# Performance work log

Measured on AMD Instinct MI355X. Metric: run time of the kernel, lower is better.

## Reference

```python
import jax, jax.numpy as jnp
import numpy as np

B, S, D = 2, 2048, 1024
N_HEADS, D_HEAD = 16, 64
INIT_STD = 0.02


def setup_inputs() -> dict:
    key = jax.random.key(0)
    k_res, k_q, k_k, k_v, k_o = jax.random.split(key, 5)
    residual = jax.random.normal(k_res, (B, S, D), dtype=jnp.float32)
    W_Q = INIT_STD * jax.random.normal(k_q, (N_HEADS, D_HEAD, D), dtype=jnp.float32)
    W_K = INIT_STD * jax.random.normal(k_k, (N_HEADS, D_HEAD, D), dtype=jnp.float32)
    W_V = INIT_STD * jax.random.normal(k_v, (N_HEADS, D_HEAD, D), dtype=jnp.float32)
    W_O = INIT_STD * jax.random.normal(k_o, (N_HEADS, D_HEAD, D), dtype=jnp.float32)
    return {"residual": residual, "W_Q": W_Q, "W_K": W_K, "W_V": W_V, "W_O": W_O}


def reference(residual, W_Q, W_K, W_V, W_O):
    seq_len = residual.shape[1]
    # projections: [b, n, p, h]  (heads first, matching q.transpose(1,2))
    q = jnp.einsum('bpd,nhd->bnph', residual, W_Q)
    k = jnp.einsum('bpd,nhd->bnph', residual, W_K)
    v = jnp.einsum('bpd,nhd->bnph', residual, W_V)
    scale = 1.0 / jnp.sqrt(jnp.asarray(q.shape[-1], dtype=residual.dtype))
    # [b, n, p_q, p_k] full score matrix (faithful to original naive impl)
    scores = jnp.einsum('bnqh,bnkh->bnqk', q, k) * scale
    causal = jnp.tril(jnp.ones((seq_len, seq_len), dtype=bool))
    scores = jnp.where(causal, scores, -jnp.inf)
    pattern = jax.nn.softmax(scores, axis=-1)
    attn_out = jnp.einsum('bnqk,bnkh->bnqh', pattern, v)
    # output projection summed over heads: 'bpnh,nhd->bpd'
    return jnp.einsum('bnph,nhd->bpd', attn_out, W_O)
```

## Files before the change

### kernel.cpp

```cpp
#include <hip/hip_runtime.h>
#include <math.h>


#define SS_ 2048
#define DD_ 1024
#define NH_ 16
#define BN_ 32
#define BS_ 4096

typedef __bf16 bf16x8 __attribute__((ext_vector_type(8)));
typedef __bf16 bf16x4 __attribute__((ext_vector_type(4)));
typedef short shortx4 __attribute__((ext_vector_type(4)));
typedef float floatx4 __attribute__((ext_vector_type(4)));
typedef unsigned short ushortx4 __attribute__((ext_vector_type(4)));

__device__ __forceinline__ unsigned short f2bf(float f) {
    union { float f; unsigned u; } v; v.f = f;
    unsigned r = v.u + 0x7FFFu + ((v.u >> 16) & 1u);
    return (unsigned short)(r >> 16);
}

__device__ __forceinline__ floatx4 mfma_pv(bf16x4 a, bf16x4 b, floatx4 c) {
#if __has_builtin(__builtin_amdgcn_mfma_f32_16x16x16_bf16)
    return __builtin_amdgcn_mfma_f32_16x16x16_bf16(a, b, c, 0, 0, 0);
#else
    return __builtin_amdgcn_mfma_f32_16x16x16bf16_1k(
        __builtin_bit_cast(shortx4, a), __builtin_bit_cast(shortx4, b), c, 0, 0, 0);
#endif
}

__device__ __forceinline__ void gl_lds16(const unsigned short* g, unsigned short* l) {
    __builtin_amdgcn_global_load_lds(
        (const __attribute__((address_space(1))) unsigned int*)g,
        (__attribute__((address_space(3))) unsigned int*)l, 16, 0, 0);
}

__global__ __launch_bounds__(256) void cast_bf16_kernel(
    const float* __restrict__ resid, const float* __restrict__ WQ,
    const float* __restrict__ WK, const float* __restrict__ WV,
    unsigned short* __restrict__ residB, unsigned short* __restrict__ WQb,
    unsigned short* __restrict__ WKb, unsigned short* __restrict__ WVb)
{
    const int x = blockIdx.x;
    int z, ix;
    if (x < 4096) { z = 0; ix = x; }
    else { z = 1 + ((x - 4096) >> 10); ix = (x - 4096) & 1023; }
    const float* src = (z == 0) ? resid : (z == 1) ? WQ : (z == 2) ? WK : WV;
    unsigned short* dst = (z == 0) ? residB : (z == 1) ? WQb : (z == 2) ? WKb : WVb;
    const int i = (ix * 256 + threadIdx.x) * 4;
    float4 f = *(const float4*)(src + i);
    ushortx4 o;
    o[0] = f2bf(f.x); o[1] = f2bf(f.y); o[2] = f2bf(f.z); o[3] = f2bf(f.w);
    *(ushortx4*)(dst + i) = o;
}

__global__ __launch_bounds__(256) void wo_transpose_kernel(
    const float* __restrict__ WO, unsigned short* __restrict__ WOt)
{
    __shared__ float t[64][65];
    const int kk0 = blockIdx.x * 64, d0 = blockIdx.y * 64;
    #pragma unroll
    for (int it = 0; it < 16; ++it) {
        int idx = it * 256 + threadIdx.x;
        int r = idx >> 6, c = idx & 63;
        t[r][c] = WO[(kk0 + r) * DD_ + d0 + c];
    }
    __syncthreads();
    #pragma unroll
    for (int it = 0; it < 16; ++it) {
        int idx = it * 256 + threadIdx.x;
        int r = idx >> 6, c = idx & 63;
        WOt[(d0 + r) * DD_ + kk0 + c] = f2bf(t[c][r]);
    }
}

__global__ __launch_bounds__(512, 4) void qkv_fused_kernel(
    const unsigned short* __restrict__ residB,
    const unsigned short* __restrict__ WQb,
    const unsigned short* __restrict__ WKb,
    const unsigned short* __restrict__ WVb,
    unsigned short* __restrict__ q, unsigned short* __restrict__ kk,
    unsigned short* __restrict__ vT)
{
    __shared__ unsigned short As[128 * 64];
    __shared__ unsigned short Bq[64 * 64];
    __shared__ unsigned short Bk[64 * 64];
    __shared__ unsigned short Bv[64 * 64];
    const int tid = threadIdx.x;
    const int l = tid & 63, w = tid >> 6;
    const int quad = l >> 4, lan = l & 15;
    const int mBase = blockIdx.x * 128;
    const int head = blockIdx.y;
    const int nBase = head * 64;

    floatx4 accQ[4], accK[4], accV[4];
    #pragma unroll
    for (int ni = 0; ni < 4; ++ni)
        #pragma unroll
        for (int i = 0; i < 4; ++i) {
            accQ[ni][i] = 0.f; accK[ni][i] = 0.f; accV[ni][i] = 0.f;
        }

    const int sr = l >> 3;
    const int sgx = ((l & 7) ^ sr) * 8;

    for (int k0 = 0; k0 < DD_; k0 += 64) {
        __syncthreads();
        gl_lds16(residB + (size_t)(mBase + w * 16 + sr) * DD_ + k0 + sgx,
                 As + (w * 16) * 64);
        gl_lds16(residB + (size_t)(mBase + w * 16 + 8 + sr) * DD_ + k0 + sgx,
                 As + (w * 16 + 8) * 64);
        gl_lds16(WQb + (size_t)(nBase + w * 8 + sr) * DD_ + k0 + sgx,
                 Bq + (w * 8) * 64);
        gl_lds16(WKb + (size_t)(nBase + w * 8 + sr) * DD_ + k0 + sgx,
                 Bk + (w * 8) * 64);
        gl_lds16(WVb + (size_t)(nBase + w * 8 + sr) * DD_ + k0 + sgx,
                 Bv + (w * 8) * 64);
        __syncthreads();
        #pragma unroll
        for (int ks = 0; ks < 2; ++ks) {
            const int fo = (((ks * 4 + quad) ^ (lan & 7)) << 3);
            bf16x8 a = *(const bf16x8*)(As + (w * 16 + lan) * 64 + fo);
            bf16x8 bq[4], bk[4], bv[4];
            #pragma unroll
            for (int ni = 0; ni < 4; ++ni) {
                bq[ni] = *(const bf16x8*)(Bq + (ni * 16 + lan) * 64 + fo);
                bk[ni] = *(const bf16x8*)(Bk + (ni * 16 + lan) * 64 + fo);
                bv[ni] = *(const bf16x8*)(Bv + (ni * 16 + lan) * 64 + fo);
            }
            #pragma unroll
            for (int ni = 0; ni < 4; ++ni) {
                accQ[ni] = __builtin_amdgcn_mfma_f32_16x16x32_bf16(a, bq[ni], accQ[ni], 0, 0, 0);
                accK[ni] = __builtin_amdgcn_mfma_f32_16x16x32_bf16(a, bk[ni], accK[ni], 0, 0, 0);
                accV[ni] = __builtin_amdgcn_mfma_f32_16x16x32_bf16(a, bv[ni], accV[ni], 0, 0, 0);
            }
        }
    }
    const int m0 = mBase + w * 16 + quad * 4;
    const int bb = m0 >> 11, ss0 = m0 & 2047;
    const float scl = 0.125f * 1.44269504088896340736f;
    #pragma unroll
    for (int ni = 0; ni < 4; ++ni) {
        const int h = ni * 16 + lan;
        bf16x4 obq, obv;
        #pragma unroll
        for (int reg = 0; reg < 4; ++reg) {
            obq[reg] = static_cast<__bf16>(accQ[ni][reg] * scl);
            obv[reg] = static_cast<__bf16>(accV[ni][reg]);
        }
        *(bf16x4*)(q  + ((size_t)(bb * NH_ + head) * 64 + h) * SS_ + ss0) = obq;
        *(bf16x4*)(vT + ((size_t)(bb * NH_ + head) * 64 + h) * SS_ + ss0) = obv;
        #pragma unroll
        for (int reg = 0; reg < 4; ++reg)
            kk[((size_t)(bb * NH_ + head) * SS_ + ss0 + reg) * 64 + h] =
                f2bf(accK[ni][reg]);
    }
}

__global__ __launch_bounds__(256, 4) void flash_mfma_kernel(
    const unsigned short* __restrict__ q,
    const unsigned short* __restrict__ k,
    const unsigned short* __restrict__ vT,
    unsigned short* __restrict__ attn)
{
    __shared__ unsigned short ldsK[2][64 * 64];
    __shared__ unsigned short ldsV[2][64 * 64];
    const int l = threadIdx.x & 63, w = threadIdx.x >> 6;
    const int quad = l >> 4, lan = l & 15;
    const int f = blockIdx.x;
    const int bn = (f & 7) | (((f >> 3) & 3) << 3);
    const int g = f >> 5;
    const int ch = (g < 8) ? (31 - g)
                 : (g < 16) ? (g + 8)
                 : (g < 24) ? (15 - (g - 16))
                 : (g - 24);

    const unsigned short* Qg = q  + (size_t)bn * 64 * SS_;
    const unsigned short* Kg = k  + (size_t)bn * SS_ * 64;
    const unsigned short* Vg = vT + (size_t)bn * 64 * SS_;

    const int srl = l >> 3;
    const int sgx = (l & 7) ^ srl;

    const int qRow0 = ch * 64 + w * 16;
    const int qAbs = qRow0 + lan;

    bf16x8 Qf0, Qf1;
    #pragma unroll
    for (int j = 0; j < 8; ++j) {
        Qf0[j] = *(const __bf16*)(Qg + (size_t)(quad * 8 + j) * SS_ + qAbs);
        Qf1[j] = *(const __bf16*)(Qg + (size_t)(quad * 8 + j + 32) * SS_ + qAbs);
    }

    bf16x4 ones;
    #pragma unroll
    for (int i = 0; i < 4; ++i) ones[i] = static_cast<__bf16>(1.0f);

    float mrow = -INFINITY;
    floatx4 l_acc;
    floatx4 o[4];
    #pragma unroll
    for (int i = 0; i < 4; ++i) l_acc[i] = 0.f;
    #pragma unroll
    for (int t = 0; t < 4; ++t)
        #pragma unroll
        for (int i = 0; i < 4; ++i) o[t][i] = 0.f;

    #define STAGE_K(kt_, buf_)                                                  \
        { const int row0_ = w * 16, kB_ = (kt_) * 64;                           \
          gl_lds16(Kg + (size_t)(kB_ + row0_ + srl) * 64 + sgx * 8,             \
                   &ldsK[buf_][row0_ * 64]);                                    \
          gl_lds16(Kg + (size_t)(kB_ + row0_ + 8 + srl) * 64 + sgx * 8,         \
                   &ldsK[buf_][(row0_ + 8) * 64]); }
    #define STAGE_V(kt_, buf_)                                                  \
        { const int row0_ = w * 16, kB_ = (kt_) * 64;                           \
          gl_lds16(Vg + (size_t)(row0_ + srl) * SS_ + kB_ + sgx * 8,            \
                   &ldsV[buf_][row0_ * 64]);                                    \
          gl_lds16(Vg + (size_t)(row0_ + 8 + srl) * SS_ + kB_ + sgx * 8,        \
                   &ldsV[buf_][(row0_ + 8) * 64]); }
    #define QK_TILE(dst_, buf_)                                                 \
        { const unsigned short* Kb_ = &ldsK[buf_][0];                           \
          bf16x8 K0v_[4], K1v_[4];                                              \
          _Pragma("unroll")                                                     \
          for (int nt = 0; nt < 4; ++nt) {                                      \
              const unsigned short* kr_ = Kb_ + (nt * 16 + lan) * 64;           \
              K0v_[nt] = *(const bf16x8*)(kr_ + ((quad ^ (lan & 7)) << 3));     \
              K1v_[nt] = *(const bf16x8*)(kr_ + (((quad + 4) ^ (lan & 7)) << 3)); } \
          _Pragma("unroll")                                                     \
          for (int nt = 0; nt < 4; ++nt) {                                      \
              floatx4 zz_; zz_[0] = zz_[1] = zz_[2] = zz_[3] = 0.f;             \
              dst_[nt] = __builtin_amdgcn_mfma_f32_16x16x32_bf16(K0v_[nt], Qf0, zz_, 0, 0, 0); \
              dst_[nt] = __builtin_amdgcn_mfma_f32_16x16x32_bf16(K1v_[nt], Qf1, dst_[nt], 0, 0, 0); } }

    STAGE_K(0, 0);
    STAGE_V(0, 0);
    __syncthreads();
    if (ch >= 1) STAGE_K(1, 1);
    floatx4 scCur[4], scNext[4];
    QK_TILE(scCur, 0);

    for (int kt = 0; kt <= ch; ++kt) {
        const int kBase = kt * 64;
        __syncthreads();
        if (kt + 2 <= ch) STAGE_K(kt + 2, (kt + 2) & 1);
        if (kt + 1 <= ch) {
            STAGE_V(kt + 1, (kt + 1) & 1);
            QK_TILE(scNext, (kt + 1) & 1);
        }
        const unsigned short* Vb = &ldsV[kt & 1][0];
        bf16x4 Vfv[4][4];
        #pragma unroll
        for (int t = 0; t < 4; ++t) {
            const unsigned short* vr = Vb + (t * 16 + lan) * 64 + ((quad & 1) << 2);
            #pragma unroll
            for (int nt = 0; nt < 4; ++nt) {
                const int g2 = nt * 2 + (quad >> 1);
                Vfv[t][nt] = *(const bf16x4*)(vr + ((g2 ^ (lan & 7)) << 3));
            }
        }
        if (kt == ch) {
            #pragma unroll
            for (int nt = 0; nt < 4; ++nt)
                #pragma unroll
                for (int reg = 0; reg < 4; ++reg)
                    if (kBase + nt * 16 + quad * 4 + reg > qAbs)
                        scCur[nt][reg] = -INFINITY;
        }
        float mx = scCur[0][0];
        #pragma unroll
        for (int nt = 0; nt < 4; ++nt)
            #pragma unroll
            for (int reg = 0; reg < 4; ++reg) mx = fmaxf(mx, scCur[nt][reg]);
        mx = fmaxf(mx, __shfl_xor(mx, 16, 64));
        mx = fmaxf(mx, __shfl_xor(mx, 32, 64));
        const float mnew = fmaxf(mrow, mx);
        if (!__all(mx <= mrow)) {
            const float alpha = exp2f(mrow - mnew);
            l_acc[0] *= alpha;
            #pragma unroll
            for (int t = 0; t < 4; ++t)
                #pragma unroll
                for (int i = 0; i < 4; ++i) o[t][i] *= alpha;
        }
        mrow = mnew;
        bf16x4 pb[4];
        #pragma unroll
        for (int nt = 0; nt < 4; ++nt)
            #pragma unroll
            for (int reg = 0; reg < 4; ++reg)
                pb[nt][reg] = static_cast<__bf16>(exp2f(scCur[nt][reg] - mnew));
        #pragma unroll
        for (int nt = 0; nt < 4; ++nt)
            l_acc = mfma_pv(ones, pb[nt], l_acc);
        #pragma unroll
        for (int t = 0; t < 4; ++t)
            #pragma unroll
            for (int nt = 0; nt < 4; ++nt)
                o[t] = mfma_pv(Vfv[t][nt], pb[nt], o[t]);
        #pragma unroll
        for (int nt = 0; nt < 4; ++nt) scCur[nt] = scNext[nt];
    }
    const float rl = 1.f / l_acc[0];
    #pragma unroll
    for (int t = 0; t < 4; ++t) {
        bf16x4 ob;
        #pragma unroll
        for (int reg = 0; reg < 4; ++reg)
            ob[reg] = static_cast<__bf16>(o[t][reg] * rl);
        *(bf16x4*)(attn + ((size_t)bn * SS_ + qAbs) * 64 + t * 16 + quad * 4) = ob;
    }
    #undef STAGE_K
    #undef STAGE_V
    #undef QK_TILE
}

__global__ __launch_bounds__(256) void out_m97_kernel(
    const unsigned short* __restrict__ attn,
    const unsigned short* __restrict__ WOt,
    float* __restrict__ out)
{
    __shared__ unsigned short As[64 * 64];
    __shared__ unsigned short Bs[128 * 64];
    const int tid = threadIdx.x;
    const int l = tid & 63, w = tid >> 6;
    const int quad = l >> 4, lan = l & 15;
    const int mBase = blockIdx.x * 64;
    const int nBase = blockIdx.y * 128;
    const int wm = (w & 1) * 32, wn = (w >> 1) * 64;
    const int bbU = mBase >> 11;
    const int ssBase = mBase & 2047;

    floatx4 acc[2][4];
    #pragma unroll
    for (int a = 0; a < 2; ++a)
        #pragma unroll
        for (int b = 0; b < 4; ++b)
            #pragma unroll
            for (int i = 0; i < 4; ++i) acc[a][b][i] = 0.f;

    const int sr = l >> 3;
    const int sgx = ((l & 7) ^ sr) * 8;

    for (int kt = 0; kt < 16; ++kt) {
        const int k0 = kt * 64;
        __syncthreads();
        #pragma unroll
        for (int i = 0; i < 2; ++i) {
            const int row = i * 32 + w * 8 + sr;
            gl_lds16(attn + ((size_t)(bbU * NH_ + kt) * SS_ + ssBase + row) * 64 + sgx,
                     As + i * 2048 + w * 512);
        }
        #pragma unroll
        for (int i = 0; i < 4; ++i) {
            const int row = i * 32 + w * 8 + sr;
            gl_lds16(WOt + (size_t)(nBase + row) * DD_ + k0 + sgx,
                     Bs + i * 2048 + w * 512);
        }
        __syncthreads();
        #pragma unroll
        for (int ks = 0; ks < 2; ++ks) {
            const int fo = (((ks * 4 + quad) ^ (lan & 7)) << 3);
            bf16x8 a[2], b[4];
            #pragma unroll
            for (int mi = 0; mi < 2; ++mi)
                a[mi] = *(const bf16x8*)(As + (wm + mi * 16 + lan) * 64 + fo);
            #pragma unroll
            for (int ni = 0; ni < 4; ++ni)
                b[ni] = *(const bf16x8*)(Bs + (wn + ni * 16 + lan) * 64 + fo);
            #pragma unroll
            for (int mi = 0; mi < 2; ++mi)
                #pragma unroll
                for (int ni = 0; ni < 4; ++ni)
                    acc[mi][ni] = __builtin_amdgcn_mfma_f32_16x16x32_bf16(
                        a[mi], b[ni], acc[mi][ni], 0, 0, 0);
        }
    }
    #pragma unroll
    for (int mi = 0; mi < 2; ++mi)
        #pragma unroll
        for (int ni = 0; ni < 4; ++ni)
            #pragma unroll
            for (int reg = 0; reg < 4; ++reg) {
                int m = mBase + wm + mi * 16 + quad * 4 + reg;
                out[(size_t)m * DD_ + nBase + wn + ni * 16 + lan] = acc[mi][ni][reg];
            }
}

extern "C" void kernel_launch(void* const* d_in, const int* in_sizes, int n_in,
                              void* d_out, int out_size, void* d_ws, size_t ws_size,
                              hipStream_t stream) {
    const float* resid = (const float*)d_in[0];
    const float* WQ    = (const float*)d_in[1];
    const float* WK    = (const float*)d_in[2];
    const float* WV    = (const float*)d_in[3];
    const float* WO    = (const float*)d_in[4];
    float* out = (float*)d_out;

    unsigned short* q      = (unsigned short*)d_ws;
    unsigned short* kk     = q      + 4194304;
    unsigned short* vT     = kk     + 4194304;
    unsigned short* attn   = vT     + 4194304;
    unsigned short* residB = attn   + 4194304;
    unsigned short* WQb    = residB + 4194304;
    unsigned short* WKb    = WQb    + 1048576;
    unsigned short* WVb    = WKb    + 1048576;
    unsigned short* WOt    = WVb    + 1048576;

    cast_bf16_kernel<<<dim3(7168), 256, 0, stream>>>(
        resid, WQ, WK, WV, residB, WQb, WKb, WVb);
    wo_transpose_kernel<<<dim3(16, 16), 256, 0, stream>>>(WO, WOt);
    qkv_fused_kernel<<<dim3(32, 16), 512, 0, stream>>>(
        residB, WQb, WKb, WVb, q, kk, vT);
    flash_mfma_kernel<<<dim3(1024), dim3(256), 0, stream>>>(q, kk, vT, attn);
    out_m97_kernel<<<dim3(64, 8), 256, 0, stream>>>(attn, WOt, out);
}
```

Baseline: 178.8 us.

## Split flash-attention KV range across two wave groups and merge softmax states

Each flash-attention block now runs 512 threads as two groups of four waves. Each group processes half of the causal key tiles for the same 64 query rows, using separate double-buffered LDS for K and V. A final merge step passes the running max, denominator and output accumulators through LDS and combines them in the log-sum-exp way. This shortens the serial loop for long-context blocks and improves load balance. The cost is double the LDS, extra synchronisation and merge overhead, and a dropped launch-bounds occupancy hint.

```diff
diff --git a/kernel.cpp b/kernel.cpp
--- a/kernel.cpp
+++ b/kernel.cpp
@@ -157,15 +157,16 @@
     }
 }
 
-__global__ __launch_bounds__(256, 4) void flash_mfma_kernel(
+__global__ __launch_bounds__(512) void flash_mfma_kernel(
     const unsigned short* __restrict__ q,
     const unsigned short* __restrict__ k,
     const unsigned short* __restrict__ vT,
     unsigned short* __restrict__ attn)
 {
-    __shared__ unsigned short ldsK[2][64 * 64];
-    __shared__ unsigned short ldsV[2][64 * 64];
+    __shared__ unsigned short ldsBuf[2][2][2][64 * 64];
     const int l = threadIdx.x & 63, w = threadIdx.x >> 6;
+    const int grp = w >> 2;
+    const int wl = w & 3;
     const int quad = l >> 4, lan = l & 15;
     const int f = blockIdx.x;
     const int bn = (f & 7) | (((f >> 3) & 3) << 3);
@@ -182,8 +183,12 @@
     const int srl = l >> 3;
     const int sgx = (l & 7) ^ srl;
 
-    const int qRow0 = ch * 64 + w * 16;
-    const int qAbs = qRow0 + lan;
+    const int qAbs = ch * 64 + wl * 16 + lan;
+
+    const int half = (ch + 1) >> 1;
+    const int base = grp ? half : 0;
+    const int cg   = grp ? (ch + 1 - half) : half;
+    const int nIt  = ch + 1 - half;
 
     bf16x8 Qf0, Qf1;
     #pragma unroll
@@ -207,19 +212,19 @@
         for (int i = 0; i < 4; ++i) o[t][i] = 0.f;
 
     #define STAGE_K(kt_, buf_)                                                  \
-        { const int row0_ = w * 16, kB_ = (kt_) * 64;                           \
+        { const int row0_ = wl * 16, kB_ = (kt_) * 64;                          \
           gl_lds16(Kg + (size_t)(kB_ + row0_ + srl) * 64 + sgx * 8,             \
-                   &ldsK[buf_][row0_ * 64]);                                    \
+                   &ldsBuf[grp][0][buf_][row0_ * 64]);                          \
           gl_lds16(Kg + (size_t)(kB_ + row0_ + 8 + srl) * 64 + sgx * 8,         \
-                   &ldsK[buf_][(row0_ + 8) * 64]); }
+                   &ldsBuf[grp][0][buf_][(row0_ + 8) * 64]); }
     #define STAGE_V(kt_, buf_)                                                  \
-        { const int row0_ = w * 16, kB_ = (kt_) * 64;                           \
+        { const int row0_ = wl * 16, kB_ = (kt_) * 64;                          \
           gl_lds16(Vg + (size_t)(row0_ + srl) * SS_ + kB_ + sgx * 8,            \
-                   &ldsV[buf_][row0_ * 64]);                                    \
+                   &ldsBuf[grp][1][buf_][row0_ * 64]);                          \
           gl_lds16(Vg + (size_t)(row0_ + 8 + srl) * SS_ + kB_ + sgx * 8,        \
-                   &ldsV[buf_][(row0_ + 8) * 64]); }
+                   &ldsBuf[grp][1][buf_][(row0_ + 8) * 64]); }
     #define QK_TILE(dst_, buf_)                                                 \
-        { const unsigned short* Kb_ = &ldsK[buf_][0];                           \
+        { const unsigned short* Kb_ = &ldsBuf[grp][0][buf_][0];                 \
           bf16x8 K0v_[4], K1v_[4];                                              \
           _Pragma("unroll")                                                     \
           for (int nt = 0; nt < 4; ++nt) {                                      \
@@ -232,86 +237,109 @@
               dst_[nt] = __builtin_amdgcn_mfma_f32_16x16x32_bf16(K0v_[nt], Qf0, zz_, 0, 0, 0); \
               dst_[nt] = __builtin_amdgcn_mfma_f32_16x16x32_bf16(K1v_[nt], Qf1, dst_[nt], 0, 0, 0); } }
 
-    STAGE_K(0, 0);
-    STAGE_V(0, 0);
+    if (cg >= 1) { STAGE_K(base, 0); STAGE_V(base, 0); }
     __syncthreads();
-    if (ch >= 1) STAGE_K(1, 1);
+    if (cg >= 2) STAGE_K(base + 1, 1);
     floatx4 scCur[4], scNext[4];
-    QK_TILE(scCur, 0);
-
-    for (int kt = 0; kt <= ch; ++kt) {
-        const int kBase = kt * 64;
+    if (cg >= 1) QK_TILE(scCur, 0);
+
+    for (int i = 0; i < nIt; ++i) {
         __syncthreads();
-        if (kt + 2 <= ch) STAGE_K(kt + 2, (kt + 2) & 1);
-        if (kt + 1 <= ch) {
-            STAGE_V(kt + 1, (kt + 1) & 1);
-            QK_TILE(scNext, (kt + 1) & 1);
-        }
-        const unsigned short* Vb = &ldsV[kt & 1][0];
-        bf16x4 Vfv[4][4];
-        #pragma unroll
-        for (int t = 0; t < 4; ++t) {
-            const unsigned short* vr = Vb + (t * 16 + lan) * 64 + ((quad & 1) << 2);
-            #pragma unroll
-            for (int nt = 0; nt < 4; ++nt) {
-                const int g2 = nt * 2 + (quad >> 1);
-                Vfv[t][nt] = *(const bf16x4*)(vr + ((g2 ^ (lan & 7)) << 3));
-            }
-        }
-        if (kt == ch) {
+        if (i < cg) {
+            const int t = base + i;
+            if (i + 2 < cg) STAGE_K(base + i + 2, (i + 2) & 1);
+            if (i + 1 < cg) {
+                STAGE_V(base + i + 1, (i + 1) & 1);
+                QK_TILE(scNext, (i + 1) & 1);
+            }
+            const unsigned short* Vb = &ldsBuf[grp][1][i & 1][0];
+            bf16x4 Vfv[4][4];
+            #pragma unroll
+            for (int tt = 0; tt < 4; ++tt) {
+                const unsigned short* vr = Vb + (tt * 16 + lan) * 64 + ((quad & 1) << 2);
+                #pragma unroll
+                for (int nt = 0; nt < 4; ++nt) {
+                    const int g2 = nt * 2 + (quad >> 1);
+                    Vfv[tt][nt] = *(const bf16x4*)(vr + ((g2 ^ (lan & 7)) << 3));
+                }
+            }
+            if (t == ch) {
+                const int kBase = t * 64;
+                #pragma unroll
+                for (int nt = 0; nt < 4; ++nt)
+                    #pragma unroll
+                    for (int reg = 0; reg < 4; ++reg)
+                        if (kBase + nt * 16 + quad * 4 + reg > qAbs)
+                            scCur[nt][reg] = -INFINITY;
+            }
+            float mx = scCur[0][0];
             #pragma unroll
             for (int nt = 0; nt < 4; ++nt)
                 #pragma unroll
+                for (int reg = 0; reg < 4; ++reg) mx = fmaxf(mx, scCur[nt][reg]);
+            mx = fmaxf(mx, __shfl_xor(mx, 16, 64));
+            mx = fmaxf(mx, __shfl_xor(mx, 32, 64));
+            const float mnew = fmaxf(mrow, mx);
+            if (!__all(mx <= mrow)) {
+                const float alpha = exp2f(mrow - mnew);
+                l_acc[0] *= alpha;
+                #pragma unroll
+                for (int tt = 0; tt < 4; ++tt)
+                    #pragma unroll
+                    for (int ii = 0; ii < 4; ++ii) o[tt][ii] *= alpha;
+            }
+            mrow = mnew;
+            bf16x4 pb[4];
+            #pragma unroll
+            for (int nt = 0; nt < 4; ++nt)
+                #pragma unroll
                 for (int reg = 0; reg < 4; ++reg)
-                    if (kBase + nt * 16 + quad * 4 + reg > qAbs)
-                        scCur[nt][reg] = -INFINITY;
-        }
-        float mx = scCur[0][0];
-        #pragma unroll
-        for (int nt = 0; nt < 4; ++nt)
-            #pragma unroll
-            for (int reg = 0; reg < 4; ++reg) mx = fmaxf(mx, scCur[nt][reg]);
-        mx = fmaxf(mx, __shfl_xor(mx, 16, 64));
-        mx = fmaxf(mx, __shfl_xor(mx, 32, 64));
-        const float mnew = fmaxf(mrow, mx);
-        if (!__all(mx <= mrow)) {
-            const float alpha = exp2f(mrow - mnew);
-            l_acc[0] *= alpha;
-            #pragma unroll
-            for (int t = 0; t < 4; ++t)
-                #pragma unroll
-                for (int i = 0; i < 4; ++i) o[t][i] *= alpha;
-        }
-        mrow = mnew;
-        bf16x4 pb[4];
-        #pragma unroll
-        for (int nt = 0; nt < 4; ++nt)
-            #pragma unroll
-            for (int reg = 0; reg < 4; ++reg)
-                pb[nt][reg] = static_cast<__bf16>(exp2f(scCur[nt][reg] - mnew));
-        #pragma unroll
-        for (int nt = 0; nt < 4; ++nt)
-            l_acc = mfma_pv(ones, pb[nt], l_acc);
-        #pragma unroll
-        for (int t = 0; t < 4; ++t)
+                    pb[nt][reg] = static_cast<__bf16>(exp2f(scCur[nt][reg] - mnew));
             #pragma unroll
             for (int nt = 0; nt < 4; ++nt)
-                o[t] = mfma_pv(Vfv[t][nt], pb[nt], o[t]);
-        #pragma unroll
-        for (int nt = 0; nt < 4; ++nt) scCur[nt] = scNext[nt];
-    }
-    const float rl = 1.f / l_acc[0];
-    #pragma unroll
-    for (int t = 0; t < 4; ++t) {
-        bf16x4 ob;
-        #pragma unroll
-        for (int reg = 0; reg < 4; ++reg)
-            ob[reg] = static_cast<__bf16>(o[t][reg] * rl);
-        *(bf16x4*)(attn + ((size_t)bn * SS_ + qAbs) * 64 + t * 16 + quad * 4) = ob;
+                l_acc = mfma_pv(ones, pb[nt], l_acc);
+            #pragma unroll
+            for (int tt = 0; tt < 4; ++tt)
+                #pragma unroll
+                for (int nt = 0; nt < 4; ++nt)
+                    o[tt] = mfma_pv(Vfv[tt][nt], pb[nt], o[tt]);
+            if (i + 1 < cg) {
+                #pragma unroll
+                for (int nt = 0; nt < 4; ++nt) scCur[nt] = scNext[nt];
+            }
+        }
     }
     #undef STAGE_K
     #undef STAGE_V
     #undef QK_TILE
+
+    __syncthreads();
+    float* scr = (float*)&ldsBuf[0][0][0][0];
+    float* s = scr + (int)threadIdx.x * 18;
+    s[0] = mrow;
+    s[1] = l_acc[0];
+    #pragma unroll
+    for (int t = 0; t < 4; ++t)
+        #pragma unroll
+        for (int reg = 0; reg < 4; ++reg) s[2 + t * 4 + reg] = o[t][reg];
+    __syncthreads();
+    if (grp == 0) {
+        const float* p = scr + ((int)threadIdx.x + 256) * 18;
+        const float m1 = p[0], l1 = p[1];
+        const float m = fmaxf(mrow, m1);
+        const float a0 = exp2f(mrow - m);
+        const float a1 = exp2f(m1 - m);
+        const float rl = 1.f / (l_acc[0] * a0 + l1 * a1);
+        #pragma unroll
+        for (int t = 0; t < 4; ++t) {
+            bf16x4 ob;
+            #pragma unroll
+            for (int reg = 0; reg < 4; ++reg)
+                ob[reg] = static_cast<__bf16>(
+                    (o[t][reg] * a0 + p[2 + t * 4 + reg] * a1) * rl);
+            *(bf16x4*)(attn + ((size_t)bn * SS_ + qAbs) * 64 + t * 16 + quad * 4) = ob;
+        }
+    }
 }
 
 __global__ __launch_bounds__(256) void out_m97_kernel(
@@ -411,6 +439,6 @@
     wo_transpose_kernel<<<dim3(16, 16), 256, 0, stream>>>(WO, WOt);
     qkv_fused_kernel<<<dim3(32, 16), 512, 0, stream>>>(
         residB, WQb, WKb, WVb, q, kk, vT);
-    flash_mfma_kernel<<<dim3(1024), dim3(256), 0, stream>>>(q, kk, vT, attn);
+    flash_mfma_kernel<<<dim3(1024), dim3(512), 0, stream>>>(q, kk, vT, attn);
     out_m97_kernel<<<dim3(64, 8), 256, 0, stream>>>(attn, WOt, out);
 }
```

Result: slower. 194.9 us (+9.0%).

## Split causal KV range into two halves per query tile with combine pass

Applied to the files above, without the earlier changes.

The flash attention grid is doubled so that each query chunk's causal KV range is split across two blocks. Each block writes an unnormalized partial output plus its row max and row sum, and a new combine kernel merges the two halves with a log-sum-exp rescale. The aim is to shorten the critical path of the longest causal chunks and to improve load balance across CUs. In exchange it adds an extra kernel launch, extra global traffic for the partial outputs, and reuses the residB and WQb workspace buffers as scratch.

```diff
diff --git a/kernel.cpp b/kernel.cpp
--- a/kernel.cpp
+++ b/kernel.cpp
@@ -161,7 +161,9 @@
     const unsigned short* __restrict__ q,
     const unsigned short* __restrict__ k,
     const unsigned short* __restrict__ vT,
-    unsigned short* __restrict__ attn)
+    unsigned short* __restrict__ pO0,
+    unsigned short* __restrict__ pO1,
+    float* __restrict__ ml)
 {
     __shared__ unsigned short ldsK[2][64 * 64];
     __shared__ unsigned short ldsV[2][64 * 64];
@@ -169,11 +171,11 @@
     const int quad = l >> 4, lan = l & 15;
     const int f = blockIdx.x;
     const int bn = (f & 7) | (((f >> 3) & 3) << 3);
-    const int g = f >> 5;
-    const int ch = (g < 8) ? (31 - g)
-                 : (g < 16) ? (g + 8)
-                 : (g < 24) ? (15 - (g - 16))
-                 : (g - 24);
+    const int ch = 31 - ((f >> 5) & 31);
+    const int half = f >> 10;
+    const int hsz = (ch + 1) >> 1;
+    const int base = half ? hsz : 0;
+    const int cnt = half ? (ch + 1 - hsz) : hsz;
 
     const unsigned short* Qg = q  + (size_t)bn * 64 * SS_;
     const unsigned short* Kg = k  + (size_t)bn * SS_ * 64;
@@ -182,8 +184,7 @@
     const int srl = l >> 3;
     const int sgx = (l & 7) ^ srl;
 
-    const int qRow0 = ch * 64 + w * 16;
-    const int qAbs = qRow0 + lan;
+    const int qAbs = ch * 64 + w * 16 + lan;
 
     bf16x8 Qf0, Qf1;
     #pragma unroll
@@ -232,33 +233,33 @@
               dst_[nt] = __builtin_amdgcn_mfma_f32_16x16x32_bf16(K0v_[nt], Qf0, zz_, 0, 0, 0); \
               dst_[nt] = __builtin_amdgcn_mfma_f32_16x16x32_bf16(K1v_[nt], Qf1, dst_[nt], 0, 0, 0); } }
 
-    STAGE_K(0, 0);
-    STAGE_V(0, 0);
+    if (cnt >= 1) { STAGE_K(base, 0); STAGE_V(base, 0); }
     __syncthreads();
-    if (ch >= 1) STAGE_K(1, 1);
+    if (cnt >= 2) STAGE_K(base + 1, 1);
     floatx4 scCur[4], scNext[4];
-    QK_TILE(scCur, 0);
-
-    for (int kt = 0; kt <= ch; ++kt) {
-        const int kBase = kt * 64;
+    if (cnt >= 1) QK_TILE(scCur, 0);
+
+    for (int i = 0; i < cnt; ++i) {
+        const int t = base + i;
         __syncthreads();
-        if (kt + 2 <= ch) STAGE_K(kt + 2, (kt + 2) & 1);
-        if (kt + 1 <= ch) {
-            STAGE_V(kt + 1, (kt + 1) & 1);
-            QK_TILE(scNext, (kt + 1) & 1);
-        }
-        const unsigned short* Vb = &ldsV[kt & 1][0];
+        if (i + 2 < cnt) STAGE_K(base + i + 2, (i + 2) & 1);
+        if (i + 1 < cnt) {
+            STAGE_V(base + i + 1, (i + 1) & 1);
+            QK_TILE(scNext, (i + 1) & 1);
+        }
+        const unsigned short* Vb = &ldsV[i & 1][0];
         bf16x4 Vfv[4][4];
         #pragma unroll
-        for (int t = 0; t < 4; ++t) {
-            const unsigned short* vr = Vb + (t * 16 + lan) * 64 + ((quad & 1) << 2);
+        for (int tt = 0; tt < 4; ++tt) {
+            const unsigned short* vr = Vb + (tt * 16 + lan) * 64 + ((quad & 1) << 2);
             #pragma unroll
             for (int nt = 0; nt < 4; ++nt) {
                 const int g2 = nt * 2 + (quad >> 1);
-                Vfv[t][nt] = *(const bf16x4*)(vr + ((g2 ^ (lan & 7)) << 3));
+                Vfv[tt][nt] = *(const bf16x4*)(vr + ((g2 ^ (lan & 7)) << 3));
             }
         }
-        if (kt == ch) {
+        if (t == ch) {
+            const int kBase = t * 64;
             #pragma unroll
             for (int nt = 0; nt < 4; ++nt)
                 #pragma unroll
@@ -278,9 +279,9 @@
             const float alpha = exp2f(mrow - mnew);
             l_acc[0] *= alpha;
             #pragma unroll
-            for (int t = 0; t < 4; ++t)
+            for (int tt = 0; tt < 4; ++tt)
                 #pragma unroll
-                for (int i = 0; i < 4; ++i) o[t][i] *= alpha;
+                for (int ii = 0; ii < 4; ++ii) o[tt][ii] *= alpha;
         }
         mrow = mnew;
         bf16x4 pb[4];
@@ -293,25 +294,59 @@
         for (int nt = 0; nt < 4; ++nt)
             l_acc = mfma_pv(ones, pb[nt], l_acc);
         #pragma unroll
-        for (int t = 0; t < 4; ++t)
+        for (int tt = 0; tt < 4; ++tt)
             #pragma unroll
             for (int nt = 0; nt < 4; ++nt)
-                o[t] = mfma_pv(Vfv[t][nt], pb[nt], o[t]);
-        #pragma unroll
-        for (int nt = 0; nt < 4; ++nt) scCur[nt] = scNext[nt];
-    }
-    const float rl = 1.f / l_acc[0];
-    #pragma unroll
-    for (int t = 0; t < 4; ++t) {
-        bf16x4 ob;
-        #pragma unroll
-        for (int reg = 0; reg < 4; ++reg)
-            ob[reg] = static_cast<__bf16>(o[t][reg] * rl);
-        *(bf16x4*)(attn + ((size_t)bn * SS_ + qAbs) * 64 + t * 16 + quad * 4) = ob;
+                o[tt] = mfma_pv(Vfv[tt][nt], pb[nt], o[tt]);
+        if (i + 1 < cnt) {
+            #pragma unroll
+            for (int nt = 0; nt < 4; ++nt) scCur[nt] = scNext[nt];
+        }
     }
     #undef STAGE_K
     #undef STAGE_V
     #undef QK_TILE
+
+    unsigned short* pO = half ? pO1 : pO0;
+    const size_t rbase = ((size_t)bn * SS_ + qAbs) * 64;
+    #pragma unroll
+    for (int t = 0; t < 4; ++t) {
+        bf16x4 ob;
+        #pragma unroll
+        for (int reg = 0; reg < 4; ++reg)
+            ob[reg] = static_cast<__bf16>(o[t][reg]);
+        *(bf16x4*)(pO + rbase + t * 16 + quad * 4) = ob;
+    }
+    if (quad == 0) {
+        float* M = ml + half * 131072;
+        M[bn * SS_ + qAbs] = mrow;
+        M[65536 + bn * SS_ + qAbs] = l_acc[0];
+    }
+}
+
+__global__ __launch_bounds__(256) void combine_kernel(
+    const unsigned short* __restrict__ pO0,
+    unsigned short* __restrict__ attn,
+    const float* __restrict__ ml)
+{
+    const int r = blockIdx.x * 256 + threadIdx.x;
+    const float m0 = ml[r],          l0 = ml[65536 + r];
+    const float m1 = ml[131072 + r], l1 = ml[196608 + r];
+    const float m = fmaxf(m0, m1);
+    const float a0 = exp2f(m0 - m), a1 = exp2f(m1 - m);
+    const float rl = 1.f / (l0 * a0 + l1 * a1);
+    const size_t bo = (size_t)r * 64;
+    #pragma unroll
+    for (int j = 0; j < 8; ++j) {
+        bf16x8 v0 = *(const bf16x8*)(pO0 + bo + j * 8);
+        bf16x8 v1 = *(const bf16x8*)(attn + bo + j * 8);
+        bf16x8 ov;
+        #pragma unroll
+        for (int e = 0; e < 8; ++e)
+            ov[e] = static_cast<__bf16>(
+                ((float)v0[e] * a0 + (float)v1[e] * a1) * rl);
+        *(bf16x8*)(attn + bo + j * 8) = ov;
+    }
 }
 
 __global__ __launch_bounds__(256) void out_m97_kernel(
@@ -411,6 +446,9 @@
     wo_transpose_kernel<<<dim3(16, 16), 256, 0, stream>>>(WO, WOt);
     qkv_fused_kernel<<<dim3(32, 16), 512, 0, stream>>>(
         residB, WQb, WKb, WVb, q, kk, vT);
-    flash_mfma_kernel<<<dim3(1024), dim3(256), 0, stream>>>(q, kk, vT, attn);
+    flash_mfma_kernel<<<dim3(2048), dim3(256), 0, stream>>>(
+        q, kk, vT, residB , attn , (float*)WQb );
+    combine_kernel<<<dim3(256), dim3(256), 0, stream>>>(
+        residB, attn, (const float*)WQb);
     out_m97_kernel<<<dim3(64, 8), 256, 0, stream>>>(attn, WOt, out);
 }
```

After: 186.3 us. 1.04x slower.
